# Performance work log

Measured on AMD Instinct MI355X. Metric: run time of the kernel, lower is better.

The kernel has to match this reference:

```python
import jax, jax.numpy as jnp
import numpy as np

B, CIN, H, W = 4, 1024, 64, 64
PLANES = 256
K = 3
DIL = 2
PAD = DIL * (K - 1) // 2  # = 2
EPS = 1e-5


def setup_inputs() -> dict:
    key = jax.random.key(0)
    ks = jax.random.split(key, 16)
    d = {}
    d['x'] = jax.random.normal(ks[0], (B, CIN, H, W), dtype=jnp.float32)
    # conv1: 1x1, inplanes->planes, no bias
    d['w1'] = jax.random.normal(ks[1], (PLANES, CIN), dtype=jnp.float32) * 0.02
    d['gamma1'] = jnp.ones((PLANES,), jnp.float32)
    d['beta1'] = jnp.zeros((PLANES,), jnp.float32)
    d['mean1'] = jax.random.normal(ks[2], (PLANES,), dtype=jnp.float32) * 0.1
    d['var1'] = jax.random.uniform(ks[3], (PLANES,), minval=0.5, maxval=1.5, dtype=jnp.float32)
    # deform_offset: 3x3 conv planes->18, with bias
    d['woff'] = jax.random.normal(ks[4], (18, PLANES, K, K), dtype=jnp.float32) * 0.01
    d['boff'] = jnp.zeros((18,), jnp.float32)
    # conv2 (deformable): 3x3 planes->planes, with bias
    d['w2'] = jax.random.normal(ks[5], (PLANES, PLANES, K, K), dtype=jnp.float32) * 0.02
    d['bconv2'] = jnp.zeros((PLANES,), jnp.float32)
    d['gamma2'] = jnp.ones((PLANES,), jnp.float32)
    d['beta2'] = jnp.zeros((PLANES,), jnp.float32)
    d['mean2'] = jax.random.normal(ks[6], (PLANES,), dtype=jnp.float32) * 0.1
    d['var2'] = jax.random.uniform(ks[7], (PLANES,), minval=0.5, maxval=1.5, dtype=jnp.float32)
    # conv3: 1x1 planes->planes*4, no bias
    d['w3'] = jax.random.normal(ks[8], (PLANES * 4, PLANES), dtype=jnp.float32) * 0.02
    d['gamma3'] = jnp.ones((PLANES * 4,), jnp.float32)
    d['beta3'] = jnp.zeros((PLANES * 4,), jnp.float32)
    d['mean3'] = jax.random.normal(ks[9], (PLANES * 4,), dtype=jnp.float32) * 0.1
    d['var3'] = jax.random.uniform(ks[10], (PLANES * 4,), minval=0.5, maxval=1.5, dtype=jnp.float32)
    return d


def _bn(x, gamma, beta, mean, var):
    # inference-mode BatchNorm over channel dim (NCHW)
    inv = jax.lax.rsqrt(var + EPS)
    return (x - mean[:, None, None]) * (inv * gamma)[:, None, None] + beta[:, None, None]


def _deform_conv(x, offset, w, b):
    # x: [B,C,H,W]; offset: [B,18,H,W] ordered (dy,dx) per kernel tap; w: [O,C,3,3]
    Bn, C, Hh, Ww = x.shape
    off = offset.reshape(Bn, K * K, 2, Hh, Ww)
    off_y, off_x = off[:, :, 0], off[:, :, 1]          # [B,9,H,W]
    kk = jnp.arange(K * K)
    base_y = (kk // K) * DIL - PAD                      # [9]
    base_x = (kk % K) * DIL - PAD
    ys = jnp.arange(Hh, dtype=x.dtype)
    xs = jnp.arange(Ww, dtype=x.dtype)
    py = base_y.astype(x.dtype)[None, :, None, None] + ys[None, None, :, None] + off_y
    px = base_x.astype(x.dtype)[None, :, None, None] + xs[None, None, None, :] + off_x

    def sample_one(img, py1, px1):
        # img [C,H,W]; py1/px1 [9,H,W] -> [C,9,H,W] bilinear with zero padding
        y0 = jnp.floor(py1)
        x0 = jnp.floor(px1)
        wy = py1 - y0
        wx = px1 - x0

        def gather(yc, xc):
            yi = yc.astype(jnp.int32)
            xi = xc.astype(jnp.int32)
            valid = ((yi >= 0) & (yi < Hh) & (xi >= 0) & (xi < Ww)).astype(img.dtype)
            yi = jnp.clip(yi, 0, Hh - 1)
            xi = jnp.clip(xi, 0, Ww - 1)
            return img[:, yi, xi] * valid[None]

        v00 = gather(y0, x0)
        v01 = gather(y0, x0 + 1)
        v10 = gather(y0 + 1, x0)
        v11 = gather(y0 + 1, x0 + 1)
        return (v00 * ((1 - wy) * (1 - wx))[None] + v01 * ((1 - wy) * wx)[None]
                + v10 * (wy * (1 - wx))[None] + v11 * (wy * wx)[None])

    sampled = jax.vmap(sample_one)(x, py, px)           # [B,C,9,H,W]
    out = jnp.einsum('bckhw,ock->bohw', sampled, w.reshape(w.shape[0], C, K * K))
    return out + b[None, :, None, None]


def reference(x, w1, gamma1, beta1, mean1, var1, woff, boff, w2, bconv2,
              gamma2, beta2, mean2, var2, w3, gamma3, beta3, mean3, var3):
    residual = x
    out = jnp.einsum('bchw,oc->bohw', x, w1)            # conv1 1x1
    out = jax.nn.relu(_bn(out, gamma1, beta1, mean1, var1))
    offset = jax.lax.conv_general_dilated(
        out, woff, window_strides=(1, 1), padding=((PAD, PAD), (PAD, PAD)),
        rhs_dilation=(DIL, DIL), dimension_numbers=('NCHW', 'OIHW', 'NCHW'))
    offset = offset + boff[None, :, None, None]
    out = _deform_conv(out, offset, w2, bconv2)
    out = jax.nn.relu(_bn(out, gamma2, beta2, mean2, var2))
    out = jnp.einsum('bchw,oc->bohw', out, w3)          # conv3 1x1
    out = _bn(out, gamma3, beta3, mean3, var3)
    return jax.nn.relu(out + residual)
```

## Files before the change

kernel.cpp:

```cpp
#include <hip/hip_runtime.h>

#define EPS_BN 1e-5f

typedef __bf16 bf16x8 __attribute__((ext_vector_type(8)));
typedef float f32x4 __attribute__((ext_vector_type(4)));

__device__ __forceinline__ unsigned short f2bf(float f) {
  union { float f; unsigned u; } v; v.f = f;
  unsigned r = v.u + 0x7fffu + ((v.u >> 16) & 1u);
  return (unsigned short)(r >> 16);
}
__device__ __forceinline__ float bf2f(unsigned short h) {
  union { unsigned u; float f; } v; v.u = ((unsigned)h) << 16;
  return v.f;
}

__global__ __launch_bounds__(256) void prep_all(
    const float* __restrict__ w1, const float* __restrict__ w2, const float* __restrict__ woff,
    const float* __restrict__ w3,
    const float* g1, const float* b1, const float* m1, const float* v1,
    const float* g2, const float* b2, const float* m2, const float* v2, const float* bconv2,
    const float* g3, const float* b3, const float* m3, const float* v3,
    unsigned short* __restrict__ w1b, unsigned short* __restrict__ w2r,
    uint4* __restrict__ act1Pz, unsigned short* __restrict__ wob,
    unsigned short* __restrict__ w3b, float* __restrict__ shift3,
    float* s1, float* h1, float* s2, float* h2) {
  int bid = blockIdx.x, tid = threadIdx.x;
  if (bid < 1024) {
    int i = bid * 256 + tid;
    w1b[i] = f2bf(w1[i]);
  } else if (bid < 3328) {
    int i = (bid - 1024) * 256 + tid;
    int o = i / 2304, r = i % 2304;
    int kk = r / 256, c = r % 256;
    w2r[i] = f2bf(w2[(size_t)o * 2304 + c * 9 + kk]);
  } else if (bid < 5640) {
    int i = (bid - 3328) * 256 + tid;
    if (i < 591872) act1Pz[i] = uint4{0, 0, 0, 0};
  } else if (bid < 5928) {
    int i = (bid - 5640) * 256 + tid;
    int o = i / 2304, r = i % 2304;
    int kk = r / 256, c = r % 256;
    wob[i] = (o < 18) ? f2bf(woff[(size_t)o * 2304 + c * 9 + kk]) : (unsigned short)0;
  } else if (bid < 6952) {
    int i = (bid - 5928) * 256 + tid;
    int o = i >> 8;
    float sc = rsqrtf(v3[o] + EPS_BN) * g3[o];
    w3b[i] = f2bf(w3[i] * sc);
  } else if (bid < 6956) {
    int c = (bid - 6952) * 256 + tid;
    float sc = rsqrtf(v3[c] + EPS_BN) * g3[c];
    shift3[c] = b3[c] - m3[c] * sc;
  } else {
    int c = tid;
    float sc1 = rsqrtf(v1[c] + EPS_BN) * g1[c];
    s1[c] = sc1; h1[c] = b1[c] - m1[c] * sc1;
    float sc2 = rsqrtf(v2[c] + EPS_BN) * g2[c];
    s2[c] = sc2; h2[c] = b2[c] + (bconv2[c] - m2[c]) * sc2;
  }
}

__global__ __launch_bounds__(256) void transpose_x(const float* __restrict__ x,
                                                   unsigned short* __restrict__ xT) {
  __shared__ float t[32][33];
  int b = blockIdx.z;
  int p0 = blockIdx.x * 32, c0 = blockIdx.y * 32;
  int tx = threadIdx.x & 31, ty = threadIdx.x >> 5;
  const float* xb = x + (size_t)b * 1024 * 4096;
#pragma unroll
  for (int j = 0; j < 4; ++j) {
    int c = c0 + ty + j * 8;
    t[ty + j * 8][tx] = xb[(size_t)c * 4096 + p0 + tx];
  }
  __syncthreads();
  unsigned short* xTb = xT + (size_t)b * 4096 * 1024;
  int pl = threadIdx.x >> 3;
  int cl = (threadIdx.x & 7) * 4;
  float v0 = t[cl][pl], v1 = t[cl + 1][pl], v2 = t[cl + 2][pl], v3 = t[cl + 3][pl];
  uint2 pk;
  pk.x = (unsigned)f2bf(v0) | ((unsigned)f2bf(v1) << 16);
  pk.y = (unsigned)f2bf(v2) | ((unsigned)f2bf(v3) << 16);
  *(uint2*)(xTb + (size_t)(p0 + pl) * 1024 + c0 + cl) = pk;
}

__global__ __launch_bounds__(256) void gemm_split(
    const unsigned short* __restrict__ A, const unsigned short* __restrict__ Bm,
    unsigned short* __restrict__ part, int M, int N, int K, int KH) {
  __shared__ __align__(16) char blob[16896];
  __shared__ __align__(16) unsigned short sA1[4096];
  __shared__ __align__(16) unsigned short sB1[4096];
  unsigned short* sA0 = (unsigned short*)blob;
  unsigned short* sB0 = (unsigned short*)(blob + 8192);
  float* tbuf = (float*)blob;
  int tid = threadIdx.x, lane = tid & 63, wv = tid >> 6;
  int z = blockIdx.z;
  int m0 = blockIdx.y * 128, n0 = blockIdx.x * 128;
  f32x4 acc[4][4] = {};
  int rowA = tid >> 2;
  int kcol = (tid & 3) * 8;
  int wm = wv & 1, wn = wv >> 1;
  int lane15 = lane & 15, quad8 = (lane >> 4) * 8, quad = lane >> 4;

#define GS_STAGE(dA, dB, K0)                                                              \
  {                                                                                       \
    int k0_ = (K0);                                                                       \
    _Pragma("unroll") for (int r = 0; r < 2; ++r) {                                       \
      const unsigned short* gp = A + (size_t)(m0 + r * 64 + rowA) * K + k0_ + kcol;       \
      __builtin_amdgcn_global_load_lds((const __attribute__((address_space(1))) void*)gp, \
          (__attribute__((address_space(3))) void*)&(dA)[r * 2048 + wv * 512], 16, 0, 0); \
    }                                                                                     \
    _Pragma("unroll") for (int r = 0; r < 2; ++r) {                                       \
      const unsigned short* gp = Bm + (size_t)(n0 + r * 64 + rowA) * K + k0_ + kcol;      \
      __builtin_amdgcn_global_load_lds((const __attribute__((address_space(1))) void*)gp, \
          (__attribute__((address_space(3))) void*)&(dB)[r * 2048 + wv * 512], 16, 0, 0); \
    }                                                                                     \
  }

#define GS_COMPUTE(dA, dB)                                                                \
  {                                                                                       \
    bf16x8 afr[4], bfr[4];                                                                \
    _Pragma("unroll") for (int mi = 0; mi < 4; ++mi)                                      \
      afr[mi] = *(const bf16x8*)&(dA)[(wm * 64 + mi * 16 + lane15) * 32 + quad8];         \
    _Pragma("unroll") for (int ni = 0; ni < 4; ++ni)                                      \
      bfr[ni] = *(const bf16x8*)&(dB)[(wn * 64 + ni * 16 + lane15) * 32 + quad8];         \
    _Pragma("unroll") for (int mi = 0; mi < 4; ++mi)                                      \
      _Pragma("unroll") for (int ni = 0; ni < 4; ++ni)                                    \
        acc[mi][ni] =                                                                     \
            __builtin_amdgcn_mfma_f32_16x16x32_bf16(afr[mi], bfr[ni], acc[mi][ni], 0, 0, 0); \
  }

  int kbase = z * KH;
  int nst = KH >> 5;
  GS_STAGE(sA0, sB0, kbase);
  for (int t = 0; t < nst; t += 2) {
    GS_STAGE(sA1, sB1, kbase + (t + 1) * 32);
    asm volatile("s_waitcnt vmcnt(4)" ::: "memory");
    __builtin_amdgcn_s_barrier();
    GS_COMPUTE(sA0, sB0);
    __builtin_amdgcn_s_barrier();
    if (t + 2 < nst) {
      GS_STAGE(sA0, sB0, kbase + (t + 2) * 32);
      asm volatile("s_waitcnt vmcnt(4)" ::: "memory");
    } else {
      asm volatile("s_waitcnt vmcnt(0)" ::: "memory");
    }
    __builtin_amdgcn_s_barrier();
    GS_COMPUTE(sA1, sB1);
    __builtin_amdgcn_s_barrier();
  }
#undef GS_STAGE
#undef GS_COMPUTE

  unsigned short* outH = part + (size_t)z * M * N;
  int trow = tid >> 3;
  int tcol16 = (tid & 7) * 16;
  int growBase = m0 + (trow >> 4) * 64 + (trow & 15);
#pragma unroll
  for (int mi = 0; mi < 4; ++mi) {
    __syncthreads();
#pragma unroll
    for (int ni = 0; ni < 4; ++ni)
#pragma unroll
      for (int reg = 0; reg < 4; ++reg)
        tbuf[(wm * 16 + quad * 4 + reg) * 132 + wn * 64 + ni * 16 + lane15] = acc[mi][ni][reg];
    __syncthreads();
    int gr = growBase + mi * 16;
    const float* lp = &tbuf[trow * 132 + tcol16];
    unsigned o[8];
#pragma unroll
    for (int j = 0; j < 8; ++j)
      o[j] = (unsigned)f2bf(lp[2 * j]) | ((unsigned)f2bf(lp[2 * j + 1]) << 16);
    unsigned short* op = outH + (size_t)gr * 256 + n0 + tcol16;
    *(uint4*)(op) = uint4{o[0], o[1], o[2], o[3]};
    *(uint4*)(op + 8) = uint4{o[4], o[5], o[6], o[7]};
  }
}

template <int NS, int PAD>
__global__ __launch_bounds__(256) void epi_bn(const unsigned short* __restrict__ part,
                                              const float* __restrict__ scale,
                                              const float* __restrict__ shift,
                                              unsigned short* __restrict__ outT,
                                              unsigned short* __restrict__ outP) {
  int gid = blockIdx.x * 256 + threadIdx.x;
  int row = gid >> 5, c0 = (gid & 31) * 8;
  float v[8] = {};
#pragma unroll
  for (int s = 0; s < NS; ++s) {
    uint4 q = *(const uint4*)(part + (size_t)s * 16384 * 256 + (size_t)row * 256 + c0);
    unsigned u[4] = {q.x, q.y, q.z, q.w};
#pragma unroll
    for (int j = 0; j < 4; ++j) {
      v[2 * j]     += bf2f((unsigned short)(u[j] & 0xffffu));
      v[2 * j + 1] += bf2f((unsigned short)(u[j] >> 16));
    }
  }
  float sc[8], sh[8];
  *(float4*)&sc[0] = *(const float4*)(scale + c0); *(float4*)&sc[4] = *(const float4*)(scale + c0 + 4);
  *(float4*)&sh[0] = *(const float4*)(shift + c0); *(float4*)&sh[4] = *(const float4*)(shift + c0 + 4);
  unsigned o[4];
#pragma unroll
  for (int j = 0; j < 4; ++j) {
    float lo = fmaxf(v[2 * j] * sc[2 * j] + sh[2 * j], 0.f);
    float hi = fmaxf(v[2 * j + 1] * sc[2 * j + 1] + sh[2 * j + 1], 0.f);
    o[j] = (unsigned)f2bf(lo) | ((unsigned)f2bf(hi) << 16);
  }
  uint4 pk{o[0], o[1], o[2], o[3]};
  *(uint4*)(outT + (size_t)row * 256 + c0) = pk;
  if constexpr (PAD) {
    int bb = row >> 12, p = row & 4095;
    *(uint4*)(outP + (((size_t)(bb * 68) + (p >> 6) + 2) * 68 + (p & 63) + 2) * 256 + c0) = pk;
  }
}

__global__ __launch_bounds__(256) void gemm_res(
    const unsigned short* __restrict__ A, const unsigned short* __restrict__ Bm,
    float* __restrict__ outp, const float* __restrict__ shift3,
    const float* __restrict__ resid, int M, int N, int K, long bStrideB, long bStrideOut) {
  __shared__ __align__(16) char blob[16896];
  __shared__ __align__(16) unsigned short sA1[4096];
  __shared__ __align__(16) unsigned short sB1[4096];
  unsigned short* sA0 = (unsigned short*)blob;
  unsigned short* sB0 = (unsigned short*)(blob + 8192);
  float* tbuf = (float*)blob;
  int tid = threadIdx.x, lane = tid & 63, wv = tid >> 6;
  int z = blockIdx.z;
  const unsigned short* Bz = Bm + (size_t)z * bStrideB;
  int m0 = blockIdx.y * 128, n0 = blockIdx.x * 128;
  f32x4 acc[4][4] = {};
  int rowA = tid >> 2;
  int kcol = (tid & 3) * 8;
  int wm = wv & 1, wn = wv >> 1;
  int lane15 = lane & 15, quad8 = (lane >> 4) * 8, quad = lane >> 4;

#define GR_STAGE(dA, dB, K0)                                                              \
  {                                                                                       \
    int k0_ = (K0);                                                                       \
    _Pragma("unroll") for (int r = 0; r < 2; ++r) {                                       \
      const unsigned short* gp = A + (size_t)(m0 + r * 64 + rowA) * K + k0_ + kcol;       \
      __builtin_amdgcn_global_load_lds((const __attribute__((address_space(1))) void*)gp, \
          (__attribute__((address_space(3))) void*)&(dA)[r * 2048 + wv * 512], 16, 0, 0); \
    }                                                                                     \
    _Pragma("unroll") for (int r = 0; r < 2; ++r) {                                       \
      const unsigned short* gp = Bz + (size_t)(n0 + r * 64 + rowA) * K + k0_ + kcol;      \
      __builtin_amdgcn_global_load_lds((const __attribute__((address_space(1))) void*)gp, \
          (__attribute__((address_space(3))) void*)&(dB)[r * 2048 + wv * 512], 16, 0, 0); \
    }                                                                                     \
  }

#define GR_COMPUTE(dA, dB)                                                                \
  {                                                                                       \
    bf16x8 afr[4], bfr[4];                                                                \
    _Pragma("unroll") for (int mi = 0; mi < 4; ++mi)                                      \
      afr[mi] = *(const bf16x8*)&(dA)[(wm * 64 + mi * 16 + lane15) * 32 + quad8];         \
    _Pragma("unroll") for (int ni = 0; ni < 4; ++ni)                                      \
      bfr[ni] = *(const bf16x8*)&(dB)[(wn * 64 + ni * 16 + lane15) * 32 + quad8];         \
    _Pragma("unroll") for (int mi = 0; mi < 4; ++mi)                                      \
      _Pragma("unroll") for (int ni = 0; ni < 4; ++ni)                                    \
        acc[mi][ni] =                                                                     \
            __builtin_amdgcn_mfma_f32_16x16x32_bf16(afr[mi], bfr[ni], acc[mi][ni], 0, 0, 0); \
  }

  int nst = K >> 5;
  GR_STAGE(sA0, sB0, 0);
  for (int t = 0; t < nst; t += 2) {
    GR_STAGE(sA1, sB1, (t + 1) * 32);
    asm volatile("s_waitcnt vmcnt(4)" ::: "memory");
    __builtin_amdgcn_s_barrier();
    GR_COMPUTE(sA0, sB0);
    __builtin_amdgcn_s_barrier();
    if (t + 2 < nst) {
      GR_STAGE(sA0, sB0, (t + 2) * 32);
      asm volatile("s_waitcnt vmcnt(4)" ::: "memory");
    } else {
      asm volatile("s_waitcnt vmcnt(0)" ::: "memory");
    }
    __builtin_amdgcn_s_barrier();
    GR_COMPUTE(sA1, sB1);
    __builtin_amdgcn_s_barrier();
  }
#undef GR_STAGE
#undef GR_COMPUTE

  float* outF = outp + (size_t)z * bStrideOut;
  const float* res = resid + (size_t)z * bStrideOut;
  int trow = tid >> 3;
  int tcol = (tid & 7) * 4;
  int growBase = m0 + (trow >> 4) * 64 + (trow & 15);
#pragma unroll
  for (int mi = 0; mi < 4; ++mi) {
    __syncthreads();
#pragma unroll
    for (int ni = 0; ni < 4; ++ni)
#pragma unroll
      for (int reg = 0; reg < 4; ++reg)
        tbuf[(wm * 16 + quad * 4 + reg) * 132 + wn * 64 + ni * 16 + lane15] = acc[mi][ni][reg];
    __syncthreads();
    int gr = growBase + mi * 16;
    float sh = shift3[gr];
    const float* rp = res + (size_t)gr * N + n0 + tcol;
    float* op = outF + (size_t)gr * N + n0 + tcol;
    const float* lp = &tbuf[trow * 132 + tcol];
#pragma unroll
    for (int j = 0; j < 4; ++j) {
      float4 rv = *(const float4*)(rp + j * 32);
      float4 lv = *(const float4*)(lp + j * 32);
      float4 ov;
      ov.x = fmaxf(lv.x + sh + rv.x, 0.f);
      ov.y = fmaxf(lv.y + sh + rv.y, 0.f);
      ov.z = fmaxf(lv.z + sh + rv.z, 0.f);
      ov.w = fmaxf(lv.w + sh + rv.w, 0.f);
      *(float4*)(op + j * 32) = ov;
    }
  }
}

__global__ __launch_bounds__(256) void off_gemm(const unsigned short* __restrict__ actP,
                                                const unsigned short* __restrict__ wob,
                                                const float* __restrict__ boff,
                                                float* __restrict__ offsP) {
  __shared__ __align__(16) unsigned short sA0[4096];
  __shared__ __align__(16) unsigned short sB0[2048];
  __shared__ __align__(16) unsigned short sA1[4096];
  __shared__ __align__(16) unsigned short sB1[2048];
  int tid = threadIdx.x, lane = tid & 63, wv = tid >> 6;
  int m0 = blockIdx.x * 64;
  int lane15 = lane & 15, quad8 = (lane >> 4) * 8;
  int rowA = tid >> 3;
  int kc = (tid & 7) * 8;

  const unsigned short* baseA[2];
#pragma unroll
  for (int r = 0; r < 2; ++r) {
    int row = m0 + r * 32 + rowA;
    int b = row >> 12, p = row & 4095;
    baseA[r] = actP + (((size_t)(b * 68) + (p >> 6) + 2) * 68 + (p & 63) + 2) * 256 + kc;
  }
  const unsigned short* baseB = wob + (size_t)rowA * 2304 + kc;

  f32x4 acc[2] = {};

#define OG_STAGE(dA, dB, S)                                                               \
  {                                                                                       \
    int s_ = (S); int kk_ = s_ >> 2; int c0_ = (s_ & 3) * 64;                             \
    long shift_ = (long)(((kk_ / 3) * 2 - 2) * 68 + ((kk_ % 3) * 2 - 2));                 \
    _Pragma("unroll") for (int r = 0; r < 2; ++r) {                                       \
      const unsigned short* gp = baseA[r] + shift_ * 256 + c0_;                           \
      __builtin_amdgcn_global_load_lds((const __attribute__((address_space(1))) void*)gp, \
          (__attribute__((address_space(3))) void*)&(dA)[r * 2048 + wv * 512], 16, 0, 0); \
    }                                                                                     \
    {                                                                                     \
      const unsigned short* gp = baseB + kk_ * 256 + c0_;                                 \
      __builtin_amdgcn_global_load_lds((const __attribute__((address_space(1))) void*)gp, \
          (__attribute__((address_space(3))) void*)&(dB)[wv * 512], 16, 0, 0);            \
    }                                                                                     \
  }

#define OG_COMPUTE(dA, dB)                                                                \
  {                                                                                       \
    bf16x8 afr[2], bfr[2][2];                                                             \
    _Pragma("unroll") for (int kq = 0; kq < 2; ++kq) {                                    \
      afr[kq] = *(const bf16x8*)&(dA)[(wv * 16 + lane15) * 64 + kq * 32 + quad8];         \
      _Pragma("unroll") for (int ni = 0; ni < 2; ++ni)                                    \
        bfr[kq][ni] = *(const bf16x8*)&(dB)[(ni * 16 + lane15) * 64 + kq * 32 + quad8];   \
    }                                                                                     \
    _Pragma("unroll") for (int kq = 0; kq < 2; ++kq)                                      \
      _Pragma("unroll") for (int ni = 0; ni < 2; ++ni)                                    \
        acc[ni] = __builtin_amdgcn_mfma_f32_16x16x32_bf16(afr[kq], bfr[kq][ni], acc[ni], 0, 0, 0); \
  }

  OG_STAGE(sA0, sB0, 0);
  for (int s = 0; s < 36; s += 2) {
    OG_STAGE(sA1, sB1, s + 1);
    asm volatile("s_waitcnt vmcnt(3)" ::: "memory");
    __builtin_amdgcn_s_barrier();
    OG_COMPUTE(sA0, sB0);
    __builtin_amdgcn_s_barrier();
    if (s + 2 < 36) {
      OG_STAGE(sA0, sB0, s + 2);
      asm volatile("s_waitcnt vmcnt(3)" ::: "memory");
    } else {
      asm volatile("s_waitcnt vmcnt(0)" ::: "memory");
    }
    __builtin_amdgcn_s_barrier();
    OG_COMPUTE(sA1, sB1);
    __builtin_amdgcn_s_barrier();
  }
#undef OG_STAGE
#undef OG_COMPUTE

#pragma unroll
  for (int ni = 0; ni < 2; ++ni) {
    int o = ni * 16 + lane15;
    if (o < 18) {
      float bo = boff[o];
#pragma unroll
      for (int reg = 0; reg < 4; ++reg) {
        int row = m0 + wv * 16 + (lane >> 4) * 4 + reg;
        offsP[(size_t)row * 18 + o] = acc[ni][reg] + bo;
      }
    }
  }
}

__global__ __launch_bounds__(256) void deform_sample(const unsigned short* __restrict__ act1T,
                                                     const float* __restrict__ offsP,
                                                     unsigned short* __restrict__ S) {
  int g = threadIdx.x >> 5, t = threadIdx.x & 31;
  int idx = blockIdx.x * 8 + g;
  int b = idx >> 12, p = idx & 4095;
  int h = p >> 6, w = p & 63;
  const unsigned short* actb = act1T + (size_t)b * 4096 * 256 + t * 8;
  unsigned short* Sp = S + (size_t)idx * 2304 + t * 8;
  float ov = (t < 18) ? offsP[(size_t)idx * 18 + t] : 0.f;
#pragma unroll
  for (int kk = 0; kk < 9; ++kk) {
    float offy = __shfl(ov, 2 * kk, 32);
    float offx = __shfl(ov, 2 * kk + 1, 32);
    float py = (float)(h + (kk / 3) * 2 - 2) + offy;
    float px = (float)(w + (kk % 3) * 2 - 2) + offx;
    float fy = floorf(py), fx = floorf(px);
    int y0 = (int)fy, x0 = (int)fx;
    float wy = py - fy, wx = px - fx;
    bool yv0 = (y0 >= 0 && y0 < 64), yv1 = (y0 >= -1 && y0 < 63);
    bool xv0 = (x0 >= 0 && x0 < 64), xv1 = (x0 >= -1 && x0 < 63);
    const unsigned short* cb = actb + (y0 * 64 + x0) * 256;
    uint4 q00{0,0,0,0}, q01{0,0,0,0}, q10{0,0,0,0}, q11{0,0,0,0};
    if (yv0 && xv0) q00 = *(const uint4*)(cb);
    if (yv0 && xv1) q01 = *(const uint4*)(cb + 256);
    if (yv1 && xv0) q10 = *(const uint4*)(cb + 64 * 256);
    if (yv1 && xv1) q11 = *(const uint4*)(cb + 64 * 256 + 256);
    float w00 = (1.f - wy) * (1.f - wx), w01 = (1.f - wy) * wx;
    float w10 = wy * (1.f - wx), w11 = wy * wx;
    unsigned u00[4] = {q00.x, q00.y, q00.z, q00.w};
    unsigned u01[4] = {q01.x, q01.y, q01.z, q01.w};
    unsigned u10[4] = {q10.x, q10.y, q10.z, q10.w};
    unsigned u11[4] = {q11.x, q11.y, q11.z, q11.w};
    unsigned out[4];
#pragma unroll
    for (int j = 0; j < 4; ++j) {
      float lo = bf2f((unsigned short)(u00[j] & 0xffffu)) * w00 +
                 bf2f((unsigned short)(u01[j] & 0xffffu)) * w01 +
                 bf2f((unsigned short)(u10[j] & 0xffffu)) * w10 +
                 bf2f((unsigned short)(u11[j] & 0xffffu)) * w11;
      float hi = bf2f((unsigned short)(u00[j] >> 16)) * w00 +
                 bf2f((unsigned short)(u01[j] >> 16)) * w01 +
                 bf2f((unsigned short)(u10[j] >> 16)) * w10 +
                 bf2f((unsigned short)(u11[j] >> 16)) * w11;
      out[j] = (unsigned)f2bf(lo) | ((unsigned)f2bf(hi) << 16);
    }
    *(uint4*)(Sp + kk * 256) = uint4{out[0], out[1], out[2], out[3]};
  }
}

extern "C" void kernel_launch(void* const* d_in, const int* in_sizes, int n_in,
                              void* d_out, int out_size, void* d_ws, size_t ws_size,
                              hipStream_t stream) {
  const float* x      = (const float*)d_in[0];
  const float* w1     = (const float*)d_in[1];
  const float* gamma1 = (const float*)d_in[2];
  const float* beta1  = (const float*)d_in[3];
  const float* mean1  = (const float*)d_in[4];
  const float* var1   = (const float*)d_in[5];
  const float* woff   = (const float*)d_in[6];
  const float* boff   = (const float*)d_in[7];
  const float* w2     = (const float*)d_in[8];
  const float* bconv2 = (const float*)d_in[9];
  const float* gamma2 = (const float*)d_in[10];
  const float* beta2  = (const float*)d_in[11];
  const float* mean2  = (const float*)d_in[12];
  const float* var2   = (const float*)d_in[13];
  const float* w3     = (const float*)d_in[14];
  const float* gamma3 = (const float*)d_in[15];
  const float* beta3  = (const float*)d_in[16];
  const float* mean3  = (const float*)d_in[17];
  const float* var3   = (const float*)d_in[18];

  char* ws = (char*)d_ws;
  unsigned short* xT    = (unsigned short*)(ws);
  unsigned short* act1T = (unsigned short*)(ws + 33554432);
  unsigned short* act2T = (unsigned short*)(ws + 41943040);
  unsigned short* S     = (unsigned short*)(ws + 50331648);
  float*          offs  = (float*)(ws + 125829120);
  unsigned short* w1b   = (unsigned short*)(ws + 127008768);
  unsigned short* w2r   = (unsigned short*)(ws + 127533056);
  unsigned short* w3b   = (unsigned short*)(ws + 128712704);
  float*          bnS1  = (float*)(ws + 129236992);
  float*          bnH1  = (float*)(ws + 129238016);
  float*          bnS2  = (float*)(ws + 129239040);
  float*          bnH2  = (float*)(ws + 129240064);
  float*          shift3= (float*)(ws + 129241088);
  unsigned short* act1P = S;
  unsigned short* part1 = (unsigned short*)(ws + 62914560);
  unsigned short* part2 = (unsigned short*)ws;
  unsigned short* wob   = act2T;

  prep_all<<<6957, 256, 0, stream>>>(w1, w2, woff, w3,
                                     gamma1, beta1, mean1, var1,
                                     gamma2, beta2, mean2, var2, bconv2,
                                     gamma3, beta3, mean3, var3,
                                     w1b, w2r, (uint4*)act1P, wob, w3b, shift3,
                                     bnS1, bnH1, bnS2, bnH2);
  transpose_x<<<dim3(128, 32, 4), 256, 0, stream>>>(x, xT);

  gemm_split<<<dim3(2, 128, 2), 256, 0, stream>>>(xT, w1b, part1, 16384, 256, 1024, 512);
  epi_bn<2, 1><<<2048, 256, 0, stream>>>(part1, bnS1, bnH1, act1T, act1P);

  off_gemm<<<256, 256, 0, stream>>>(act1P, wob, boff, offs);
  deform_sample<<<dim3(2048), 256, 0, stream>>>(act1T, offs, S);

  gemm_split<<<dim3(2, 128, 2), 256, 0, stream>>>(S, w2r, part2, 16384, 256, 2304, 1152);
  epi_bn<2, 0><<<2048, 256, 0, stream>>>(part2, bnS2, bnH2, act2T, nullptr);

  gemm_res<<<dim3(32, 8, 4), 256, 0, stream>>>(w3b, act2T, (float*)d_out, shift3, x,
                                               1024, 4096, 256, 4096L * 256, 4194304L);
}
```

Measured before the change: 285.1 us.

## Fuse deformable bilinear sampling into the conv2 GEMM A-tile loader

Removes the separate deform_sample kernel and its large im2col buffer S, which was written to global memory and read back by the split-K GEMM. The new gemm_deform computes the bilinear-interpolated A tiles on the fly from act1T into double-buffered shared memory, while B tiles stream in through global_load_lds. Split-K changes from 2 to 3 so that each z slice covers three kernel taps, and the epilogue reduces three partials. This saves the HBM traffic for S, at the cost of recomputing the gathers once per N-block (two blocks) and more register pressure in the GEMM loop.

```diff
diff --git a/kernel.cpp b/kernel.cpp
--- a/kernel.cpp
+++ b/kernel.cpp
@@ -403,53 +403,183 @@
   }
 }
 
-__global__ __launch_bounds__(256) void deform_sample(const unsigned short* __restrict__ act1T,
-                                                     const float* __restrict__ offsP,
-                                                     unsigned short* __restrict__ S) {
-  int g = threadIdx.x >> 5, t = threadIdx.x & 31;
-  int idx = blockIdx.x * 8 + g;
-  int b = idx >> 12, p = idx & 4095;
-  int h = p >> 6, w = p & 63;
-  const unsigned short* actb = act1T + (size_t)b * 4096 * 256 + t * 8;
-  unsigned short* Sp = S + (size_t)idx * 2304 + t * 8;
-  float ov = (t < 18) ? offsP[(size_t)idx * 18 + t] : 0.f;
-#pragma unroll
-  for (int kk = 0; kk < 9; ++kk) {
-    float offy = __shfl(ov, 2 * kk, 32);
-    float offx = __shfl(ov, 2 * kk + 1, 32);
-    float py = (float)(h + (kk / 3) * 2 - 2) + offy;
-    float px = (float)(w + (kk % 3) * 2 - 2) + offx;
-    float fy = floorf(py), fx = floorf(px);
-    int y0 = (int)fy, x0 = (int)fx;
-    float wy = py - fy, wx = px - fx;
-    bool yv0 = (y0 >= 0 && y0 < 64), yv1 = (y0 >= -1 && y0 < 63);
-    bool xv0 = (x0 >= 0 && x0 < 64), xv1 = (x0 >= -1 && x0 < 63);
-    const unsigned short* cb = actb + (y0 * 64 + x0) * 256;
-    uint4 q00{0,0,0,0}, q01{0,0,0,0}, q10{0,0,0,0}, q11{0,0,0,0};
-    if (yv0 && xv0) q00 = *(const uint4*)(cb);
-    if (yv0 && xv1) q01 = *(const uint4*)(cb + 256);
-    if (yv1 && xv0) q10 = *(const uint4*)(cb + 64 * 256);
-    if (yv1 && xv1) q11 = *(const uint4*)(cb + 64 * 256 + 256);
-    float w00 = (1.f - wy) * (1.f - wx), w01 = (1.f - wy) * wx;
-    float w10 = wy * (1.f - wx), w11 = wy * wx;
-    unsigned u00[4] = {q00.x, q00.y, q00.z, q00.w};
-    unsigned u01[4] = {q01.x, q01.y, q01.z, q01.w};
-    unsigned u10[4] = {q10.x, q10.y, q10.z, q10.w};
-    unsigned u11[4] = {q11.x, q11.y, q11.z, q11.w};
-    unsigned out[4];
-#pragma unroll
-    for (int j = 0; j < 4; ++j) {
-      float lo = bf2f((unsigned short)(u00[j] & 0xffffu)) * w00 +
-                 bf2f((unsigned short)(u01[j] & 0xffffu)) * w01 +
-                 bf2f((unsigned short)(u10[j] & 0xffffu)) * w10 +
-                 bf2f((unsigned short)(u11[j] & 0xffffu)) * w11;
-      float hi = bf2f((unsigned short)(u00[j] >> 16)) * w00 +
-                 bf2f((unsigned short)(u01[j] >> 16)) * w01 +
-                 bf2f((unsigned short)(u10[j] >> 16)) * w10 +
-                 bf2f((unsigned short)(u11[j] >> 16)) * w11;
-      out[j] = (unsigned)f2bf(lo) | ((unsigned)f2bf(hi) << 16);
-    }
-    *(uint4*)(Sp + kk * 256) = uint4{out[0], out[1], out[2], out[3]};
+struct Geom { float w00, w01, w10, w11; int b00, b01, b10, b11; };
+
+__device__ __forceinline__ Geom make_geom(const float* __restrict__ offs, int row, int h, int w, int kk) {
+  float offy = offs[(size_t)row * 18 + 2 * kk];
+  float offx = offs[(size_t)row * 18 + 2 * kk + 1];
+  float py = (float)(h + (kk / 3) * 2 - 2) + offy;
+  float px = (float)(w + (kk % 3) * 2 - 2) + offx;
+  float fy = floorf(py), fx = floorf(px);
+  int y0 = (int)fy, x0 = (int)fx;
+  float wy = py - fy, wx = px - fx;
+  bool yv0 = (y0 >= 0 && y0 < 64), yv1 = (y0 >= -1 && y0 < 63);
+  bool xv0 = (x0 >= 0 && x0 < 64), xv1 = (x0 >= -1 && x0 < 63);
+  Geom g;
+  g.w00 = (yv0 && xv0) ? (1.f - wy) * (1.f - wx) : 0.f;
+  g.w01 = (yv0 && xv1) ? (1.f - wy) * wx : 0.f;
+  g.w10 = (yv1 && xv0) ? wy * (1.f - wx) : 0.f;
+  g.w11 = (yv1 && xv1) ? wy * wx : 0.f;
+  int y0c = min(max(y0, 0), 63), y1c = min(max(y0 + 1, 0), 63);
+  int x0c = min(max(x0, 0), 63), x1c = min(max(x0 + 1, 0), 63);
+  g.b00 = (y0c * 64 + x0c) * 256; g.b01 = (y0c * 64 + x1c) * 256;
+  g.b10 = (y1c * 64 + x0c) * 256; g.b11 = (y1c * 64 + x1c) * 256;
+  return g;
+}
+
+__global__ __launch_bounds__(256, 3) void gemm_deform(
+    const unsigned short* __restrict__ act1T, const float* __restrict__ offs,
+    const unsigned short* __restrict__ Bm, unsigned short* __restrict__ part) {
+  __shared__ __align__(16) char blob[16896];
+  __shared__ __align__(16) unsigned short sA1[4096];
+  __shared__ __align__(16) unsigned short sB1[4096];
+  unsigned short* sA0 = (unsigned short*)blob;
+  unsigned short* sB0 = (unsigned short*)(blob + 8192);
+  float* tbuf = (float*)blob;
+  int tid = threadIdx.x, lane = tid & 63, wv = tid >> 6;
+  int z = blockIdx.z;
+  int m0 = blockIdx.y * 128, n0 = blockIdx.x * 128;
+  f32x4 acc[4][4] = {};
+  int rowB = tid >> 2, kcolB = (tid & 3) * 8;
+  int rowl = tid >> 1, halfc = tid & 1;
+  int row = m0 + rowl;
+  int b = row >> 12, p = row & 4095, h = p >> 6, w = p & 63;
+  const unsigned short* actb = act1T + (size_t)b * 1048576 + halfc * 16;
+  int wm = wv & 1, wn = wv >> 1;
+  int lane15 = lane & 15, quad8 = (lane >> 4) * 8, quad = lane >> 4;
+
+  Geom g0 = make_geom(offs, row, h, w, 3 * z + 0);
+  Geom g1 = make_geom(offs, row, h, w, 3 * z + 1);
+  Geom g2 = make_geom(offs, row, h, w, 3 * z + 2);
+
+  uint4 rc0, rc1, rc2, rc3, rc4, rc5, rc6, rc7;
+
+#define DF_ISSUE_A(G, CS)                                                                 \
+  {                                                                                       \
+    const unsigned short* pa = actb + (CS) * 32;                                          \
+    rc0 = *(const uint4*)(pa + (G).b00); rc1 = *(const uint4*)(pa + (G).b00 + 8);         \
+    rc2 = *(const uint4*)(pa + (G).b01); rc3 = *(const uint4*)(pa + (G).b01 + 8);         \
+    rc4 = *(const uint4*)(pa + (G).b10); rc5 = *(const uint4*)(pa + (G).b10 + 8);         \
+    rc6 = *(const uint4*)(pa + (G).b11); rc7 = *(const uint4*)(pa + (G).b11 + 8);         \
+  }
+
+#define DF_ISSUE_B(DB, BCOL)                                                              \
+  {                                                                                       \
+    _Pragma("unroll") for (int r = 0; r < 2; ++r) {                                       \
+      const unsigned short* gp = Bm + (size_t)(n0 + r * 64 + rowB) * 2304 + (BCOL) + kcolB; \
+      __builtin_amdgcn_global_load_lds((const __attribute__((address_space(1))) void*)gp, \
+          (__attribute__((address_space(3))) void*)&(DB)[r * 2048 + wv * 512], 16, 0, 0); \
+    }                                                                                     \
+  }
+
+#define DF_LERP_WRITE(G, DA)                                                              \
+  {                                                                                       \
+    unsigned u00[8] = {rc0.x, rc0.y, rc0.z, rc0.w, rc1.x, rc1.y, rc1.z, rc1.w};           \
+    unsigned u01[8] = {rc2.x, rc2.y, rc2.z, rc2.w, rc3.x, rc3.y, rc3.z, rc3.w};           \
+    unsigned u10[8] = {rc4.x, rc4.y, rc4.z, rc4.w, rc5.x, rc5.y, rc5.z, rc5.w};           \
+    unsigned u11[8] = {rc6.x, rc6.y, rc6.z, rc6.w, rc7.x, rc7.y, rc7.z, rc7.w};           \
+    unsigned o8[8];                                                                       \
+    _Pragma("unroll") for (int j = 0; j < 8; ++j) {                                       \
+      float lo = bf2f((unsigned short)(u00[j] & 0xffffu)) * (G).w00 +                     \
+                 bf2f((unsigned short)(u01[j] & 0xffffu)) * (G).w01 +                     \
+                 bf2f((unsigned short)(u10[j] & 0xffffu)) * (G).w10 +                     \
+                 bf2f((unsigned short)(u11[j] & 0xffffu)) * (G).w11;                      \
+      float hi = bf2f((unsigned short)(u00[j] >> 16)) * (G).w00 +                         \
+                 bf2f((unsigned short)(u01[j] >> 16)) * (G).w01 +                         \
+                 bf2f((unsigned short)(u10[j] >> 16)) * (G).w10 +                         \
+                 bf2f((unsigned short)(u11[j] >> 16)) * (G).w11;                          \
+      o8[j] = (unsigned)f2bf(lo) | ((unsigned)f2bf(hi) << 16);                            \
+    }                                                                                     \
+    unsigned short* wp = (DA) + rowl * 32 + halfc * 16;                                   \
+    *(uint4*)(wp) = uint4{o8[0], o8[1], o8[2], o8[3]};                                    \
+    *(uint4*)(wp + 8) = uint4{o8[4], o8[5], o8[6], o8[7]};                                \
+  }
+
+#define DF_COMPUTE(DA, DB)                                                                \
+  {                                                                                       \
+    bf16x8 afr[4], bfr[4];                                                                \
+    _Pragma("unroll") for (int mi = 0; mi < 4; ++mi)                                      \
+      afr[mi] = *(const bf16x8*)&(DA)[(wm * 64 + mi * 16 + lane15) * 32 + quad8];         \
+    _Pragma("unroll") for (int ni = 0; ni < 4; ++ni)                                      \
+      bfr[ni] = *(const bf16x8*)&(DB)[(wn * 64 + ni * 16 + lane15) * 32 + quad8];         \
+    _Pragma("unroll") for (int mi = 0; mi < 4; ++mi)                                      \
+      _Pragma("unroll") for (int ni = 0; ni < 4; ++ni)                                    \
+        acc[mi][ni] =                                                                     \
+            __builtin_amdgcn_mfma_f32_16x16x32_bf16(afr[mi], bfr[ni], acc[mi][ni], 0, 0, 0); \
+  }
+
+#define DF_BC(J, CS) ((3 * z + (J)) * 256 + (CS) * 32)
+
+#define DF_BODY(GN, CSN, BCN, AC, BMC, AN, BMN)                                           \
+  {                                                                                       \
+    DF_ISSUE_A(GN, CSN);                                                                  \
+    DF_ISSUE_B(BMN, BCN);                                                                 \
+    asm volatile("s_waitcnt vmcnt(10)" ::: "memory");                                     \
+    asm volatile("s_waitcnt lgkmcnt(0)" ::: "memory");                                    \
+    __builtin_amdgcn_s_barrier();                                                         \
+    DF_COMPUTE(AC, BMC);                                                                  \
+    asm volatile("s_waitcnt vmcnt(2)" ::: "memory");                                      \
+    DF_LERP_WRITE(GN, AN);                                                                \
+    __builtin_amdgcn_s_barrier();                                                         \
+  }
+
+  DF_ISSUE_A(g0, 0);
+  DF_ISSUE_B(sB0, DF_BC(0, 0));
+  asm volatile("s_waitcnt vmcnt(2)" ::: "memory");
+  DF_LERP_WRITE(g0, sA0);
+
+  for (int cs = 0; cs < 6; cs += 2) {
+    DF_BODY(g0, cs + 1, DF_BC(0, cs + 1), sA0, sB0, sA1, sB1);
+    DF_BODY(g0, cs + 2, DF_BC(0, cs + 2), sA1, sB1, sA0, sB0);
+  }
+  DF_BODY(g0, 7, DF_BC(0, 7), sA0, sB0, sA1, sB1);
+  DF_BODY(g1, 0, DF_BC(1, 0), sA1, sB1, sA0, sB0);
+  for (int cs = 0; cs < 6; cs += 2) {
+    DF_BODY(g1, cs + 1, DF_BC(1, cs + 1), sA0, sB0, sA1, sB1);
+    DF_BODY(g1, cs + 2, DF_BC(1, cs + 2), sA1, sB1, sA0, sB0);
+  }
+  DF_BODY(g1, 7, DF_BC(1, 7), sA0, sB0, sA1, sB1);
+  DF_BODY(g2, 0, DF_BC(2, 0), sA1, sB1, sA0, sB0);
+  for (int cs = 0; cs < 6; cs += 2) {
+    DF_BODY(g2, cs + 1, DF_BC(2, cs + 1), sA0, sB0, sA1, sB1);
+    DF_BODY(g2, cs + 2, DF_BC(2, cs + 2), sA1, sB1, sA0, sB0);
+  }
+  DF_BODY(g2, 7, DF_BC(2, 7), sA0, sB0, sA1, sB1);
+  asm volatile("s_waitcnt vmcnt(0)" ::: "memory");
+  asm volatile("s_waitcnt lgkmcnt(0)" ::: "memory");
+  __builtin_amdgcn_s_barrier();
+  DF_COMPUTE(sA1, sB1);
+  __builtin_amdgcn_s_barrier();
+
+#undef DF_ISSUE_A
+#undef DF_ISSUE_B
+#undef DF_LERP_WRITE
+#undef DF_COMPUTE
+#undef DF_BC
+#undef DF_BODY
+
+  unsigned short* outH = part + (size_t)z * 16384 * 256;
+  int trow = tid >> 3;
+  int tcol16 = (tid & 7) * 16;
+  int growBase = m0 + (trow >> 4) * 64 + (trow & 15);
+#pragma unroll
+  for (int mi = 0; mi < 4; ++mi) {
+    __syncthreads();
+#pragma unroll
+    for (int ni = 0; ni < 4; ++ni)
+#pragma unroll
+      for (int reg = 0; reg < 4; ++reg)
+        tbuf[(wm * 16 + quad * 4 + reg) * 132 + wn * 64 + ni * 16 + lane15] = acc[mi][ni][reg];
+    __syncthreads();
+    int gr = growBase + mi * 16;
+    const float* lp = &tbuf[trow * 132 + tcol16];
+    unsigned o[8];
+#pragma unroll
+    for (int j = 0; j < 8; ++j)
+      o[j] = (unsigned)f2bf(lp[2 * j]) | ((unsigned)f2bf(lp[2 * j + 1]) << 16);
+    unsigned short* op = outH + (size_t)gr * 256 + n0 + tcol16;
+    *(uint4*)(op) = uint4{o[0], o[1], o[2], o[3]};
+    *(uint4*)(op + 8) = uint4{o[4], o[5], o[6], o[7]};
   }
 }
 
@@ -480,7 +610,6 @@
   unsigned short* xT    = (unsigned short*)(ws);
   unsigned short* act1T = (unsigned short*)(ws + 33554432);
   unsigned short* act2T = (unsigned short*)(ws + 41943040);
-  unsigned short* S     = (unsigned short*)(ws + 50331648);
   float*          offs  = (float*)(ws + 125829120);
   unsigned short* w1b   = (unsigned short*)(ws + 127008768);
   unsigned short* w2r   = (unsigned short*)(ws + 127533056);
@@ -490,7 +619,7 @@
   float*          bnS2  = (float*)(ws + 129239040);
   float*          bnH2  = (float*)(ws + 129240064);
   float*          shift3= (float*)(ws + 129241088);
-  unsigned short* act1P = S;
+  unsigned short* act1P = (unsigned short*)(ws + 50331648);
   unsigned short* part1 = (unsigned short*)(ws + 62914560);
   unsigned short* part2 = (unsigned short*)ws;
   unsigned short* wob   = act2T;
@@ -507,10 +636,9 @@
   epi_bn<2, 1><<<2048, 256, 0, stream>>>(part1, bnS1, bnH1, act1T, act1P);
 
   off_gemm<<<256, 256, 0, stream>>>(act1P, wob, boff, offs);
-  deform_sample<<<dim3(2048), 256, 0, stream>>>(act1T, offs, S);
-
-  gemm_split<<<dim3(2, 128, 2), 256, 0, stream>>>(S, w2r, part2, 16384, 256, 2304, 1152);
-  epi_bn<2, 0><<<2048, 256, 0, stream>>>(part2, bnS2, bnH2, act2T, nullptr);
+
+  gemm_deform<<<dim3(2, 128, 3), 256, 0, stream>>>(act1T, offs, w2r, part2);
+  epi_bn<3, 0><<<2048, 256, 0, stream>>>(part2, bnS2, bnH2, act2T, nullptr);
 
   gemm_res<<<dim3(32, 8, 4), 256, 0, stream>>>(w3b, act2T, (float*)d_out, shift3, x,
                                                1024, 4096, 256, 4096L * 256, 4194304L);
```

New measurement: 304.6 us. 1.07x slower.

## Fuse x transpose and bf16 conversion into the conv1 GEMM A-tile load

Applied to the files above, without the earlier changes.

Removes the separate transpose_x kernel and the bf16 xT buffer. A new GEMM kernel reads x directly in NCHW fp32 with coalesced per-channel loads, converts to bf16 in registers, and writes transposed tiles into LDS while B is fetched via global_load_lds. This cuts a full read/write pass over x and one launch, at the cost of reading fp32 A twice (once per N-block) and higher register use.

```diff
diff --git a/kernel.cpp b/kernel.cpp
--- a/kernel.cpp
+++ b/kernel.cpp
@@ -60,27 +60,123 @@
   }
 }
 
-__global__ __launch_bounds__(256) void transpose_x(const float* __restrict__ x,
-                                                   unsigned short* __restrict__ xT) {
-  __shared__ float t[32][33];
-  int b = blockIdx.z;
-  int p0 = blockIdx.x * 32, c0 = blockIdx.y * 32;
-  int tx = threadIdx.x & 31, ty = threadIdx.x >> 5;
-  const float* xb = x + (size_t)b * 1024 * 4096;
-#pragma unroll
-  for (int j = 0; j < 4; ++j) {
-    int c = c0 + ty + j * 8;
-    t[ty + j * 8][tx] = xb[(size_t)c * 4096 + p0 + tx];
-  }
-  __syncthreads();
-  unsigned short* xTb = xT + (size_t)b * 4096 * 1024;
-  int pl = threadIdx.x >> 3;
-  int cl = (threadIdx.x & 7) * 4;
-  float v0 = t[cl][pl], v1 = t[cl + 1][pl], v2 = t[cl + 2][pl], v3 = t[cl + 3][pl];
-  uint2 pk;
-  pk.x = (unsigned)f2bf(v0) | ((unsigned)f2bf(v1) << 16);
-  pk.y = (unsigned)f2bf(v2) | ((unsigned)f2bf(v3) << 16);
-  *(uint2*)(xTb + (size_t)(p0 + pl) * 1024 + c0 + cl) = pk;
+__global__ __launch_bounds__(256) void gemm1_x(
+    const float* __restrict__ x, const unsigned short* __restrict__ Bm,
+    unsigned short* __restrict__ part, int KH) {
+  __shared__ __align__(16) char blob[16896];
+  __shared__ __align__(16) unsigned short sA1[4096];
+  __shared__ __align__(16) unsigned short sB1[4096];
+  unsigned short* sA0 = (unsigned short*)blob;
+  unsigned short* sB0 = (unsigned short*)(blob + 8192);
+  float* tbuf = (float*)blob;
+  int tid = threadIdx.x, lane = tid & 63, wv = tid >> 6;
+  int z = blockIdx.z;
+  int m0 = blockIdx.y * 128, n0 = blockIdx.x * 128;
+  f32x4 acc[4][4] = {};
+  int rowB = tid >> 2, kcolB = (tid & 3) * 8;
+  int px = tid & 127, c16 = (tid >> 7) * 16;
+  int bb = m0 >> 12, p0 = m0 & 4095;
+  const float* xa = x + (size_t)bb * 4194304 + (size_t)c16 * 4096 + (p0 + px);
+  int wm = wv & 1, wn = wv >> 1;
+  int lane15 = lane & 15, quad8 = (lane >> 4) * 8, quad = lane >> 4;
+
+  float va[16];
+
+#define G1_ISSUE_A(K0)                                                                    \
+  {                                                                                       \
+    const float* xp = xa + (size_t)(K0) * 4096;                                           \
+    _Pragma("unroll") for (int j = 0; j < 16; ++j) va[j] = xp[(size_t)j * 4096];          \
+  }
+
+#define G1_ISSUE_B(DB, K0)                                                                \
+  {                                                                                       \
+    _Pragma("unroll") for (int r = 0; r < 2; ++r) {                                       \
+      const unsigned short* gp = Bm + (size_t)(n0 + r * 64 + rowB) * 1024 + (K0) + kcolB; \
+      __builtin_amdgcn_global_load_lds((const __attribute__((address_space(1))) void*)gp, \
+          (__attribute__((address_space(3))) void*)&(DB)[r * 2048 + wv * 512], 16, 0, 0); \
+    }                                                                                     \
+  }
+
+#define G1_CVT_WRITE(DA)                                                                  \
+  {                                                                                       \
+    unsigned o8[8];                                                                       \
+    _Pragma("unroll") for (int j = 0; j < 8; ++j)                                         \
+      o8[j] = (unsigned)f2bf(va[2 * j]) | ((unsigned)f2bf(va[2 * j + 1]) << 16);          \
+    unsigned short* wp = (DA) + px * 32 + c16;                                            \
+    *(uint4*)(wp) = uint4{o8[0], o8[1], o8[2], o8[3]};                                    \
+    *(uint4*)(wp + 8) = uint4{o8[4], o8[5], o8[6], o8[7]};                                \
+  }
+
+#define G1_COMPUTE(DA, DB)                                                                \
+  {                                                                                       \
+    bf16x8 afr[4], bfr[4];                                                                \
+    _Pragma("unroll") for (int mi = 0; mi < 4; ++mi)                                      \
+      afr[mi] = *(const bf16x8*)&(DA)[(wm * 64 + mi * 16 + lane15) * 32 + quad8];         \
+    _Pragma("unroll") for (int ni = 0; ni < 4; ++ni)                                      \
+      bfr[ni] = *(const bf16x8*)&(DB)[(wn * 64 + ni * 16 + lane15) * 32 + quad8];         \
+    _Pragma("unroll") for (int mi = 0; mi < 4; ++mi)                                      \
+      _Pragma("unroll") for (int ni = 0; ni < 4; ++ni)                                    \
+        acc[mi][ni] =                                                                     \
+            __builtin_amdgcn_mfma_f32_16x16x32_bf16(afr[mi], bfr[ni], acc[mi][ni], 0, 0, 0); \
+  }
+
+#define G1_BODY(K0, AC, BC, AN, BN_)                                                      \
+  {                                                                                       \
+    G1_ISSUE_A(K0);                                                                       \
+    G1_ISSUE_B(BN_, K0);                                                                  \
+    asm volatile("s_waitcnt vmcnt(18)" ::: "memory");                                     \
+    asm volatile("s_waitcnt lgkmcnt(0)" ::: "memory");                                    \
+    __builtin_amdgcn_s_barrier();                                                         \
+    G1_COMPUTE(AC, BC);                                                                   \
+    asm volatile("s_waitcnt vmcnt(2)" ::: "memory");                                      \
+    G1_CVT_WRITE(AN);                                                                     \
+    __builtin_amdgcn_s_barrier();                                                         \
+  }
+
+  int kbase = z * KH;
+  int nst = KH >> 5;
+  G1_ISSUE_A(kbase);
+  G1_ISSUE_B(sB0, kbase);
+  asm volatile("s_waitcnt vmcnt(2)" ::: "memory");
+  G1_CVT_WRITE(sA0);
+  for (int t = 0; t + 2 < nst; t += 2) {
+    G1_BODY(kbase + (t + 1) * 32, sA0, sB0, sA1, sB1);
+    G1_BODY(kbase + (t + 2) * 32, sA1, sB1, sA0, sB0);
+  }
+  G1_BODY(kbase + (nst - 1) * 32, sA0, sB0, sA1, sB1);
+  asm volatile("s_waitcnt vmcnt(0)" ::: "memory");
+  asm volatile("s_waitcnt lgkmcnt(0)" ::: "memory");
+  __builtin_amdgcn_s_barrier();
+  G1_COMPUTE(sA1, sB1);
+#undef G1_ISSUE_A
+#undef G1_ISSUE_B
+#undef G1_CVT_WRITE
+#undef G1_COMPUTE
+#undef G1_BODY
+
+  unsigned short* outH = part + (size_t)z * 16384 * 256;
+  int trow = tid >> 3;
+  int tcol16 = (tid & 7) * 16;
+  int growBase = m0 + (trow >> 4) * 64 + (trow & 15);
+#pragma unroll
+  for (int mi = 0; mi < 4; ++mi) {
+    __syncthreads();
+#pragma unroll
+    for (int ni = 0; ni < 4; ++ni)
+#pragma unroll
+      for (int reg = 0; reg < 4; ++reg)
+        tbuf[(wm * 16 + quad * 4 + reg) * 132 + wn * 64 + ni * 16 + lane15] = acc[mi][ni][reg];
+    __syncthreads();
+    int gr = growBase + mi * 16;
+    const float* lp = &tbuf[trow * 132 + tcol16];
+    unsigned o[8];
+#pragma unroll
+    for (int j = 0; j < 8; ++j)
+      o[j] = (unsigned)f2bf(lp[2 * j]) | ((unsigned)f2bf(lp[2 * j + 1]) << 16);
+    unsigned short* op = outH + (size_t)gr * 256 + n0 + tcol16;
+    *(uint4*)(op) = uint4{o[0], o[1], o[2], o[3]};
+    *(uint4*)(op + 8) = uint4{o[4], o[5], o[6], o[7]};
+  }
 }
 
 __global__ __launch_bounds__(256) void gemm_split(
@@ -477,7 +573,6 @@
   const float* var3   = (const float*)d_in[18];
 
   char* ws = (char*)d_ws;
-  unsigned short* xT    = (unsigned short*)(ws);
   unsigned short* act1T = (unsigned short*)(ws + 33554432);
   unsigned short* act2T = (unsigned short*)(ws + 41943040);
   unsigned short* S     = (unsigned short*)(ws + 50331648);
@@ -501,9 +596,8 @@
                                      gamma3, beta3, mean3, var3,
                                      w1b, w2r, (uint4*)act1P, wob, w3b, shift3,
                                      bnS1, bnH1, bnS2, bnH2);
-  transpose_x<<<dim3(128, 32, 4), 256, 0, stream>>>(x, xT);
-
-  gemm_split<<<dim3(2, 128, 2), 256, 0, stream>>>(xT, w1b, part1, 16384, 256, 1024, 512);
+
+  gemm1_x<<<dim3(2, 128, 2), 256, 0, stream>>>(x, w1b, part1, 512);
   epi_bn<2, 1><<<2048, 256, 0, stream>>>(part1, bnS1, bnH1, act1T, act1P);
 
   off_gemm<<<256, 256, 0, stream>>>(act1P, wob, boff, offs);
```

New measurement: 280.5 us. Within noise of the previous version (-1.6%).
